# Performance work log

Measured on AMD Instinct MI355X. Metric: run time of the kernel, lower is better.

The kernel has to match this reference:

```python
import jax, jax.numpy as jnp
import numpy as np

B = 8        # graphs per batch
VG = 20000   # vertices per graph
K = 128      # eigenvectors per graph
D = 128      # channels (C_inout)
V = B * VG


def setup_inputs() -> dict:
    key = jax.random.key(0)
    kx, km, ke, kv, kt = jax.random.split(key, 5)
    x = jax.random.normal(kx, (V, D), dtype=jnp.float32)
    # lumped (diagonal) mass, positive
    mass = jax.random.uniform(km, (V,), dtype=jnp.float32, minval=0.5, maxval=1.5)
    # per-graph nonnegative eigenvalues, sorted within each graph, stacked to (B*K,)
    evals = jnp.sort(jax.random.uniform(ke, (B, K), dtype=jnp.float32) * 10.0, axis=1).reshape(-1)
    # eigenbasis, roughly mass-orthonormal scale
    evecs = jax.random.normal(kv, (V, K), dtype=jnp.float32) / np.sqrt(VG)
    # learned per-channel diffusion times, positive
    diffusion_time = jax.random.uniform(kt, (D,), dtype=jnp.float32, minval=0.01, maxval=0.2)
    batch = jnp.repeat(jnp.arange(B, dtype=jnp.int32), VG)
    return {"x": x, "mass": mass, "evals": evals, "evecs": evecs,
            "diffusion_time": diffusion_time, "batch": batch, "bs": B}


def reference(x, mass, evals, evecs, diffusion_time, batch, bs):
    Vtot, Dc = x.shape
    neig = evals.shape[0] // bs
    vg = Vtot // bs  # equal-sized graphs -> ragged grouped matmul == batched matmul
    t = jnp.maximum(diffusion_time, 1e-8)  # torch clamp(min=1e-8)
    xb = x.reshape(bs, vg, Dc)            # (B, Vg, D)
    eb = evecs.reshape(bs, vg, neig)      # (B, Vg, K)
    mb = mass.reshape(bs, vg)             # (B, Vg) diagonal mass
    # to_basis: basis^T @ (M x) per graph -> (B, K, D)
    x_spec = jnp.einsum('bvk,bvd->bkd', eb * mb[..., None], xb)
    # spectral diffusion coefficients exp(-lambda * t_c): (B, K, D)
    coefs = jnp.exp(-evals.reshape(bs, neig)[..., None] * t[None, None, :])
    # from_basis: evecs @ (coefs * x_spec) per graph -> (B, Vg, D)
    x_diffuse = jnp.einsum('bvk,bkd->bvd', eb, coefs * x_spec)
    return x_diffuse.reshape(Vtot, Dc)
```

## Files before the change

### kernel.cpp

```cpp
#include <hip/hip_runtime.h>

#define BGR 8
#define VG  20000
#define NK  128
#define ND  128

typedef float f32x4 __attribute__((ext_vector_type(4)));
typedef short bf16x8 __attribute__((ext_vector_type(8)));

__device__ __forceinline__ unsigned short bf16r(float f) {
    union { float f; unsigned u; } c; c.f = f;
    return (unsigned short)((c.u + 0x7FFFu + ((c.u >> 16) & 1u)) >> 16);
}
__device__ __forceinline__ unsigned pack2(float a, float b) {
    return (unsigned)bf16r(a) | ((unsigned)bf16r(b) << 16);
}

#define VC 160
#define S1 40

__global__ __launch_bounds__(256) void k_spec(const float* __restrict__ x,
                                              const float* __restrict__ mass,
                                              const float* __restrict__ evecs,
                                              float* __restrict__ xs) {
    const int g  = blockIdx.y;
    const int v0 = blockIdx.x * VC;

    const float* xg = x     + (size_t)g * VG * ND;
    const float* eg = evecs + (size_t)g * VG * NK;
    const float* mg = mass  + (size_t)g * VG;

    __shared__ short At[NK * S1];
    __shared__ short Bt[ND * S1];

    const int tid = threadIdx.x;
    const int l   = tid & 63;
    const int w   = tid >> 6;
    const int lo  = l & 15, hi = l >> 4;
    const int r0  = (w & 1) * 64, c0 = (w >> 1) * 64;

    f32x4 acc[4][4] = {};

#pragma unroll 1
    for (int r = 0; r < VC / 32; ++r) {
        const int vb = v0 + r * 32;
#pragma unroll
        for (int it = 0; it < 2; ++it) {
            const int id = it * 256 + tid;
            const int vp = id & 15;
            const int cq = id >> 4;
            const int v  = vb + 2 * vp;
            const float2 mm = *(const float2*)(mg + v);
            const f32x4 xa = *(const f32x4*)(xg + (size_t)v * ND + 4 * cq);
            const f32x4 xb = *(const f32x4*)(xg + (size_t)(v + 1) * ND + 4 * cq);
            const f32x4 ea = *(const f32x4*)(eg + (size_t)v * NK + 4 * cq);
            const f32x4 eb = *(const f32x4*)(eg + (size_t)(v + 1) * NK + 4 * cq);
#pragma unroll
            for (int i = 0; i < 4; ++i) {
                const int c = 4 * cq + i;
                *(unsigned*)(Bt + c * S1 + 2 * vp) = pack2(xa[i] * mm.x, xb[i] * mm.y);
                *(unsigned*)(At + c * S1 + 2 * vp) = pack2(ea[i], eb[i]);
            }
        }
        __syncthreads();

        bf16x8 af[4], bfv[4];
#pragma unroll
        for (int i = 0; i < 4; ++i)
            af[i] = *(const bf16x8*)(At + (r0 + 16 * i + lo) * S1 + hi * 8);
#pragma unroll
        for (int j = 0; j < 4; ++j)
            bfv[j] = *(const bf16x8*)(Bt + (c0 + 16 * j + lo) * S1 + hi * 8);
#pragma unroll
        for (int i = 0; i < 4; ++i)
#pragma unroll
            for (int j = 0; j < 4; ++j)
                acc[i][j] = __builtin_amdgcn_mfma_f32_16x16x32_bf16(af[i], bfv[j], acc[i][j], 0, 0, 0);
        __syncthreads();
    }

    float* og = xs + (size_t)g * NK * ND;
#pragma unroll
    for (int i = 0; i < 4; ++i)
#pragma unroll
        for (int j = 0; j < 4; ++j)
#pragma unroll
            for (int t = 0; t < 4; ++t) {
                const int kk = r0 + 16 * i + hi * 4 + t;
                const int dd = c0 + 16 * j + lo;
                atomicAdd(og + kk * ND + dd, acc[i][j][t]);
            }
}

__global__ __launch_bounds__(256) void k_coef(const float* __restrict__ xs,
                                              const float* __restrict__ evals,
                                              const float* __restrict__ dt,
                                              unsigned short* __restrict__ Yt) {
    const int gid = blockIdx.x * 256 + threadIdx.x;
    const int g = gid >> 14;
    const int d = (gid >> 7) & 127;
    const int k = gid & 127;
    const float t   = fmaxf(dt[d], 1e-8f);
    const float lam = evals[g * NK + k];
    const float v   = xs[(size_t)g * NK * ND + k * ND + d];
    Yt[gid] = bf16r(__expf(-lam * t) * v);
}

#define S2 136

__global__ __launch_bounds__(256) void k_out(const float* __restrict__ evecs,
                                             const short* __restrict__ Yt,
                                             float* __restrict__ out) {
    const int g     = blockIdx.y;
    const int chunk = blockIdx.x;
    const int v0    = chunk * 128;
    const int rows  = (VG - v0 < 128) ? (VG - v0) : 128;

    const float* eg = evecs + (size_t)g * VG * NK;
    float*       og = out   + (size_t)g * VG * ND;
    const short* yg = Yt    + (size_t)g * ND * NK;

    __shared__ short As[128 * S2];

    const int tid = threadIdx.x;
#pragma unroll
    for (int it = 0; it < 16; ++it) {
        const int id = it * 256 + tid;
        const int v  = id >> 5;
        const int c4 = id & 31;
        const int vc = v < rows ? v : rows - 1;
        const f32x4 e4 = *(const f32x4*)(eg + (size_t)(v0 + vc) * NK + 4 * c4);
        short4 p;
        p.x = (short)bf16r(e4.x); p.y = (short)bf16r(e4.y);
        p.z = (short)bf16r(e4.z); p.w = (short)bf16r(e4.w);
        *(short4*)(As + v * S2 + 4 * c4) = p;
    }
    __syncthreads();

    const int l  = tid & 63;
    const int w  = tid >> 6;
    const int lo = l & 15, hi = l >> 4;
    const int r0 = (w & 1) * 64, c0 = (w >> 1) * 64;

    f32x4 acc[4][4] = {};
#pragma unroll
    for (int ks = 0; ks < 4; ++ks) {
        const int k0 = ks * 32;
        bf16x8 af[4], bfv[4];
#pragma unroll
        for (int j = 0; j < 4; ++j)
            bfv[j] = *(const bf16x8*)(yg + (size_t)(c0 + 16 * j + lo) * NK + k0 + hi * 8);
#pragma unroll
        for (int i = 0; i < 4; ++i)
            af[i] = *(const bf16x8*)(As + (r0 + 16 * i + lo) * S2 + k0 + hi * 8);
#pragma unroll
        for (int i = 0; i < 4; ++i)
#pragma unroll
            for (int j = 0; j < 4; ++j)
                acc[i][j] = __builtin_amdgcn_mfma_f32_16x16x32_bf16(af[i], bfv[j], acc[i][j], 0, 0, 0);
    }

#pragma unroll
    for (int i = 0; i < 4; ++i)
#pragma unroll
        for (int j = 0; j < 4; ++j)
#pragma unroll
            for (int t = 0; t < 4; ++t) {
                const int vv = r0 + 16 * i + hi * 4 + t;
                if (vv < rows)
                    og[(size_t)(v0 + vv) * ND + c0 + 16 * j + lo] = acc[i][j][t];
            }
}

extern "C" void kernel_launch(void* const* d_in, const int* in_sizes, int n_in,
                              void* d_out, int out_size, void* d_ws, size_t ws_size,
                              hipStream_t stream) {
    const float* x     = (const float*)d_in[0];
    const float* mass  = (const float*)d_in[1];
    const float* evals = (const float*)d_in[2];
    const float* evecs = (const float*)d_in[3];
    const float* dt    = (const float*)d_in[4];
    float* out = (float*)d_out;

    float*          xs = (float*)d_ws;
    unsigned short* Yt = (unsigned short*)((char*)d_ws + (size_t)BGR * NK * ND * 4);

    hipMemsetAsync(d_ws, 0, (size_t)BGR * NK * ND * sizeof(float), stream);

    k_spec<<<dim3(VG / VC, BGR), 256, 0, stream>>>(x, mass, evecs, xs);
    k_coef<<<(BGR * NK * ND) / 256, 256, 0, stream>>>(xs, evals, dt, Yt);
    k_out<<<dim3((VG + 127) / 128, BGR), 256, 0, stream>>>(evecs, (const short*)Yt, out);
}
```

Measured before the change: 279.6 us.

## Drop LDS staging, load MFMA fragments from global, replace atomics with partial reduction

```diff
diff --git a/kernel.cpp b/kernel.cpp
--- a/kernel.cpp
+++ b/kernel.cpp
@@ -4,6 +4,8 @@
 #define VG  20000
 #define NK  128
 #define ND  128
+#define VC  320
+#define NB  ((VG + VC - 1) / VC)
 
 typedef float f32x4 __attribute__((ext_vector_type(4)));
 typedef short bf16x8 __attribute__((ext_vector_type(8)));
@@ -16,70 +18,71 @@
     return (unsigned)bf16r(a) | ((unsigned)bf16r(b) << 16);
 }
 
-#define VC 160
-#define S1 40
-
-__global__ __launch_bounds__(256) void k_spec(const float* __restrict__ x,
-                                              const float* __restrict__ mass,
-                                              const float* __restrict__ evecs,
-                                              float* __restrict__ xs) {
+template<int ATOMIC>
+__global__ __launch_bounds__(256, 2) void k_spec(const float* __restrict__ x,
+                                                 const float* __restrict__ mass,
+                                                 const float* __restrict__ evecs,
+                                                 float* __restrict__ P) {
     const int g  = blockIdx.y;
-    const int v0 = blockIdx.x * VC;
+    const int b  = blockIdx.x;
+    const int v0 = b * VC;
+    const int rounds = ((VG - v0 < VC) ? (VG - v0) : VC) >> 5;
 
     const float* xg = x     + (size_t)g * VG * ND;
     const float* eg = evecs + (size_t)g * VG * NK;
     const float* mg = mass  + (size_t)g * VG;
 
-    __shared__ short At[NK * S1];
-    __shared__ short Bt[ND * S1];
-
     const int tid = threadIdx.x;
-    const int l   = tid & 63;
-    const int w   = tid >> 6;
-    const int lo  = l & 15, hi = l >> 4;
-    const int r0  = (w & 1) * 64, c0 = (w >> 1) * 64;
+    const int l  = tid & 63, w = tid >> 6;
+    const int lo = l & 15, hi = l >> 4;
+    const int r0 = (w & 1) * 64, c0 = (w >> 1) * 64;
 
     f32x4 acc[4][4] = {};
 
 #pragma unroll 1
-    for (int r = 0; r < VC / 32; ++r) {
-        const int vb = v0 + r * 32;
+    for (int r = 0; r < rounds; ++r) {
+        const int vb = v0 + r * 32 + hi * 8;
+
+        float mj[8], ta[4][8], tb[4][8];
 #pragma unroll
-        for (int it = 0; it < 2; ++it) {
-            const int id = it * 256 + tid;
-            const int vp = id & 15;
-            const int cq = id >> 4;
-            const int v  = vb + 2 * vp;
-            const float2 mm = *(const float2*)(mg + v);
-            const f32x4 xa = *(const f32x4*)(xg + (size_t)v * ND + 4 * cq);
-            const f32x4 xb = *(const f32x4*)(xg + (size_t)(v + 1) * ND + 4 * cq);
-            const f32x4 ea = *(const f32x4*)(eg + (size_t)v * NK + 4 * cq);
-            const f32x4 eb = *(const f32x4*)(eg + (size_t)(v + 1) * NK + 4 * cq);
+        for (int jj = 0; jj < 8; ++jj) mj[jj] = mg[vb + jj];
 #pragma unroll
-            for (int i = 0; i < 4; ++i) {
-                const int c = 4 * cq + i;
-                *(unsigned*)(Bt + c * S1 + 2 * vp) = pack2(xa[i] * mm.x, xb[i] * mm.y);
-                *(unsigned*)(At + c * S1 + 2 * vp) = pack2(ea[i], eb[i]);
-            }
-        }
-        __syncthreads();
+        for (int i = 0; i < 4; ++i)
+#pragma unroll
+            for (int jj = 0; jj < 8; ++jj)
+                ta[i][jj] = eg[(size_t)(vb + jj) * NK + r0 + 16 * i + lo];
+#pragma unroll
+        for (int j = 0; j < 4; ++j)
+#pragma unroll
+            for (int jj = 0; jj < 8; ++jj)
+                tb[j][jj] = xg[(size_t)(vb + jj) * ND + c0 + 16 * j + lo];
 
         bf16x8 af[4], bfv[4];
 #pragma unroll
-        for (int i = 0; i < 4; ++i)
-            af[i] = *(const bf16x8*)(At + (r0 + 16 * i + lo) * S1 + hi * 8);
+        for (int i = 0; i < 4; ++i) {
+            union { bf16x8 v; unsigned u[4]; } a;
 #pragma unroll
-        for (int j = 0; j < 4; ++j)
-            bfv[j] = *(const bf16x8*)(Bt + (c0 + 16 * j + lo) * S1 + hi * 8);
+            for (int q = 0; q < 4; ++q)
+                a.u[q] = pack2(ta[i][2 * q], ta[i][2 * q + 1]);
+            af[i] = a.v;
+        }
+#pragma unroll
+        for (int j = 0; j < 4; ++j) {
+            union { bf16x8 v; unsigned u[4]; } bv;
+#pragma unroll
+            for (int q = 0; q < 4; ++q)
+                bv.u[q] = pack2(tb[j][2 * q] * mj[2 * q], tb[j][2 * q + 1] * mj[2 * q + 1]);
+            bfv[j] = bv.v;
+        }
 #pragma unroll
         for (int i = 0; i < 4; ++i)
 #pragma unroll
             for (int j = 0; j < 4; ++j)
                 acc[i][j] = __builtin_amdgcn_mfma_f32_16x16x32_bf16(af[i], bfv[j], acc[i][j], 0, 0, 0);
-        __syncthreads();
     }
 
-    float* og = xs + (size_t)g * NK * ND;
+    float* og = ATOMIC ? (P + ((size_t)g << 14))
+                       : (P + ((size_t)(g * NB + b) << 14));
 #pragma unroll
     for (int i = 0; i < 4; ++i)
 #pragma unroll
@@ -88,88 +91,82 @@
             for (int t = 0; t < 4; ++t) {
                 const int kk = r0 + 16 * i + hi * 4 + t;
                 const int dd = c0 + 16 * j + lo;
-                atomicAdd(og + kk * ND + dd, acc[i][j][t]);
+                if (ATOMIC) atomicAdd(og + kk * ND + dd, acc[i][j][t]);
+                else        og[kk * ND + dd] = acc[i][j][t];
             }
 }
 
-__global__ __launch_bounds__(256) void k_coef(const float* __restrict__ xs,
-                                              const float* __restrict__ evals,
-                                              const float* __restrict__ dt,
-                                              unsigned short* __restrict__ Yt) {
+template<int NPART>
+__global__ __launch_bounds__(256) void k_red(const float* __restrict__ P,
+                                             const float* __restrict__ evals,
+                                             const float* __restrict__ dt,
+                                             unsigned short* __restrict__ Yt) {
     const int gid = blockIdx.x * 256 + threadIdx.x;
-    const int g = gid >> 14;
-    const int d = (gid >> 7) & 127;
-    const int k = gid & 127;
-    const float t   = fmaxf(dt[d], 1e-8f);
-    const float lam = evals[g * NK + k];
-    const float v   = xs[(size_t)g * NK * ND + k * ND + d];
-    Yt[gid] = bf16r(__expf(-lam * t) * v);
+    const int g = gid >> 14, k = (gid >> 7) & 127, d = gid & 127;
+    const float* p = P + (((size_t)g * NPART) << 14) + (k << 7) + d;
+    float s = 0.f;
+#pragma unroll 4
+    for (int b = 0; b < NPART; ++b) s += p[(size_t)b << 14];
+    const float t = fmaxf(dt[d], 1e-8f);
+    s *= __expf(-evals[g * NK + k] * t);
+    Yt[((size_t)g << 14) + (d << 7) + k] = bf16r(s);
 }
 
-#define S2 136
-
-__global__ __launch_bounds__(256) void k_out(const float* __restrict__ evecs,
-                                             const short* __restrict__ Yt,
-                                             float* __restrict__ out) {
-    const int g     = blockIdx.y;
-    const int chunk = blockIdx.x;
-    const int v0    = chunk * 128;
-    const int rows  = (VG - v0 < 128) ? (VG - v0) : 128;
+__global__ __launch_bounds__(256, 2) void k_out(const float* __restrict__ evecs,
+                                                const unsigned short* __restrict__ Yt,
+                                                float* __restrict__ out) {
+    const int g    = blockIdx.y;
+    const int v0   = blockIdx.x * 128;
+    const int rows = (VG - v0 < 128) ? (VG - v0) : 128;
 
     const float* eg = evecs + (size_t)g * VG * NK;
     float*       og = out   + (size_t)g * VG * ND;
-    const short* yg = Yt    + (size_t)g * ND * NK;
-
-    __shared__ short As[128 * S2];
+    const unsigned short* yg = Yt + ((size_t)g << 14);
 
     const int tid = threadIdx.x;
+    const int l  = tid & 63, w = tid >> 6;
+    const int lo = l & 15, hi = l >> 4;
+    const int vr = w * 32;
+
+    f32x4 acc[2][8] = {};
+
+#pragma unroll 2
+    for (int ks = 0; ks < 4; ++ks) {
+        const int k0 = ks * 32 + hi * 8;
+
+        bf16x8 bfv[8], af[2];
 #pragma unroll
-    for (int it = 0; it < 16; ++it) {
-        const int id = it * 256 + tid;
-        const int v  = id >> 5;
-        const int c4 = id & 31;
-        const int vc = v < rows ? v : rows - 1;
-        const f32x4 e4 = *(const f32x4*)(eg + (size_t)(v0 + vc) * NK + 4 * c4);
-        short4 p;
-        p.x = (short)bf16r(e4.x); p.y = (short)bf16r(e4.y);
-        p.z = (short)bf16r(e4.z); p.w = (short)bf16r(e4.w);
-        *(short4*)(As + v * S2 + 4 * c4) = p;
-    }
-    __syncthreads();
-
-    const int l  = tid & 63;
-    const int w  = tid >> 6;
-    const int lo = l & 15, hi = l >> 4;
-    const int r0 = (w & 1) * 64, c0 = (w >> 1) * 64;
-
-    f32x4 acc[4][4] = {};
+        for (int j = 0; j < 8; ++j)
+            bfv[j] = *(const bf16x8*)(yg + (size_t)(16 * j + lo) * NK + k0);
 #pragma unroll
-    for (int ks = 0; ks < 4; ++ks) {
-        const int k0 = ks * 32;
-        bf16x8 af[4], bfv[4];
+        for (int i = 0; i < 2; ++i) {
+            int rr = vr + 16 * i + lo;
+            rr = (rr < rows) ? rr : (rows - 1);
+            const f32x4 e0 = *(const f32x4*)(eg + (size_t)(v0 + rr) * NK + k0);
+            const f32x4 e1 = *(const f32x4*)(eg + (size_t)(v0 + rr) * NK + k0 + 4);
+            union { bf16x8 v; unsigned u[4]; } a;
+            a.u[0] = pack2(e0.x, e0.y); a.u[1] = pack2(e0.z, e0.w);
+            a.u[2] = pack2(e1.x, e1.y); a.u[3] = pack2(e1.z, e1.w);
+            af[i] = a.v;
+        }
 #pragma unroll
-        for (int j = 0; j < 4; ++j)
-            bfv[j] = *(const bf16x8*)(yg + (size_t)(c0 + 16 * j + lo) * NK + k0 + hi * 8);
+        for (int i = 0; i < 2; ++i)
 #pragma unroll
-        for (int i = 0; i < 4; ++i)
-            af[i] = *(const bf16x8*)(As + (r0 + 16 * i + lo) * S2 + k0 + hi * 8);
-#pragma unroll
-        for (int i = 0; i < 4; ++i)
-#pragma unroll
-            for (int j = 0; j < 4; ++j)
+            for (int j = 0; j < 8; ++j)
                 acc[i][j] = __builtin_amdgcn_mfma_f32_16x16x32_bf16(af[i], bfv[j], acc[i][j], 0, 0, 0);
     }
 
 #pragma unroll
-    for (int i = 0; i < 4; ++i)
+    for (int i = 0; i < 2; ++i)
 #pragma unroll
-        for (int j = 0; j < 4; ++j)
+        for (int t = 0; t < 4; ++t) {
+            const int rr = vr + 16 * i + hi * 4 + t;
+            if (rr < rows) {
 #pragma unroll
-            for (int t = 0; t < 4; ++t) {
-                const int vv = r0 + 16 * i + hi * 4 + t;
-                if (vv < rows)
-                    og[(size_t)(v0 + vv) * ND + c0 + 16 * j + lo] = acc[i][j][t];
+                for (int j = 0; j < 8; ++j)
+                    og[(size_t)(v0 + rr) * ND + 16 * j + lo] = acc[i][j][t];
             }
+        }
 }
 
 extern "C" void kernel_launch(void* const* d_in, const int* in_sizes, int n_in,
@@ -182,12 +179,21 @@
     const float* dt    = (const float*)d_in[4];
     float* out = (float*)d_out;
 
-    float*          xs = (float*)d_ws;
-    unsigned short* Yt = (unsigned short*)((char*)d_ws + (size_t)BGR * NK * ND * 4);
+    const size_t pelems = (size_t)BGR * NB * NK * ND;
+    const size_t need   = pelems * 4 + (size_t)BGR * NK * ND * 2;
 
-    hipMemsetAsync(d_ws, 0, (size_t)BGR * NK * ND * sizeof(float), stream);
-
-    k_spec<<<dim3(VG / VC, BGR), 256, 0, stream>>>(x, mass, evecs, xs);
-    k_coef<<<(BGR * NK * ND) / 256, 256, 0, stream>>>(xs, evals, dt, Yt);
-    k_out<<<dim3((VG + 127) / 128, BGR), 256, 0, stream>>>(evecs, (const short*)Yt, out);
+    if (ws_size >= need) {
+        float*          P  = (float*)d_ws;
+        unsigned short* Yt = (unsigned short*)((char*)d_ws + pelems * 4);
+        k_spec<0><<<dim3(NB, BGR), 256, 0, stream>>>(x, mass, evecs, P);
+        k_red<NB><<<(BGR * NK * ND) / 256, 256, 0, stream>>>(P, evals, dt, Yt);
+        k_out<<<dim3((VG + 127) / 128, BGR), 256, 0, stream>>>(evecs, Yt, out);
+    } else {
+        float*          P  = (float*)d_ws;
+        unsigned short* Yt = (unsigned short*)((char*)d_ws + (size_t)BGR * NK * ND * 4);
+        hipMemsetAsync(P, 0, (size_t)BGR * NK * ND * sizeof(float), stream);
+        k_spec<1><<<dim3(NB, BGR), 256, 0, stream>>>(x, mass, evecs, P);
+        k_red<1><<<(BGR * NK * ND) / 256, 256, 0, stream>>>(P, evals, dt, Yt);
+        k_out<<<dim3((VG + 127) / 128, BGR), 256, 0, stream>>>(evecs, Yt, out);
+    }
 }
```

After: 263.8 us. 5.6% less time.
